# Kernel optimization log

Measured on AMD Instinct MI355X. Metric: run time of the kernel, lower is better.

Reference implementation:

```python
import jax, jax.numpy as jnp
import numpy as np

N = 100000      # nodes
E = 1600000     # edges (before self-loops)
IN_C = 128
HID = 32
HEADS = 4
NEG_SLOPE = 0.2  # PyG GATConv default


def gat_layer(x, W, a_src, a_dst, b, src, dst, n, heads, out_c, concat):
    # x: [n, F_in], W: [F_in, heads*out_c]
    h = (x @ W).reshape(n, heads, out_c)                      # [n, H, C]
    as_n = (h * a_src).sum(-1)                                # [n, H]
    ad_n = (h * a_dst).sum(-1)                                # [n, H]
    e = jax.nn.leaky_relu(as_n[src] + ad_n[dst], NEG_SLOPE)   # [E, H]
    # softmax over incoming edges of each destination node
    m = jax.ops.segment_max(e, dst, num_segments=n)           # [n, H]
    ee = jnp.exp(e - m[dst])
    denom = jax.ops.segment_sum(ee, dst, num_segments=n)      # [n, H]
    alpha = ee / (denom[dst] + 1e-16)                         # [E, H]
    out = jax.ops.segment_sum(h[src] * alpha[:, :, None], dst, num_segments=n)  # [n, H, C]
    out = out.reshape(n, heads * out_c) if concat else out.mean(axis=1)
    return out + b


def setup_inputs() -> dict:
    key = jax.random.key(0)
    ks = jax.random.split(key, 12)
    x = jax.random.normal(ks[0], (N, IN_C), dtype=jnp.float32)
    edge_index = jax.random.randint(ks[1], (2, E), 0, N, dtype=jnp.int64)
    s = 0.1
    return {
        "x": x,
        "edge_index": edge_index,
        "w1": jax.random.normal(ks[2], (IN_C, HEADS * HID), dtype=jnp.float32) * s,
        "a1_src": jax.random.normal(ks[3], (HEADS, HID), dtype=jnp.float32) * s,
        "a1_dst": jax.random.normal(ks[4], (HEADS, HID), dtype=jnp.float32) * s,
        "b1": jnp.zeros((HEADS * HID,), dtype=jnp.float32),
        "w2": jax.random.normal(ks[5], (HEADS * HID, HID), dtype=jnp.float32) * s,
        "a2_src": jax.random.normal(ks[6], (1, HID), dtype=jnp.float32) * s,
        "a2_dst": jax.random.normal(ks[7], (1, HID), dtype=jnp.float32) * s,
        "b2": jnp.zeros((HID,), dtype=jnp.float32),
        "wl": jax.random.normal(ks[8], (HID, 1), dtype=jnp.float32) * s,
        "bl": jnp.zeros((1,), dtype=jnp.float32),
    }


def reference(x, edge_index, w1, a1_src, a1_dst, b1, w2, a2_src, a2_dst, b2, wl, bl):
    n = x.shape[0]
    loop = jnp.arange(n, dtype=edge_index.dtype)
    # PyG GATConv adds self-loops by default
    src = jnp.concatenate([edge_index[0], loop])
    dst = jnp.concatenate([edge_index[1], loop])
    h = jax.nn.elu(gat_layer(x, w1, a1_src, a1_dst, b1, src, dst, n, HEADS, HID, True))
    h = jax.nn.elu(gat_layer(h, w2, a2_src, a2_dst, b2, src, dst, n, 1, HID, False))
    return (h @ wl + bl).squeeze(-1)   # [n]
```

## Files before the change

### kernel.cpp

```cpp
#include <hip/hip_runtime.h>
#include <math.h>

__device__ __forceinline__ float leaky02(float v) { return v > 0.f ? v : 0.2f * v; }
__device__ __forceinline__ float eluf(float v) { return v > 0.f ? v : __expf(v) - 1.f; }
__device__ __forceinline__ float expc(float v) { return __expf(fminf(v, 60.f)); }
__device__ __forceinline__ unsigned short f2bf(float f) {
    unsigned int u = __float_as_uint(f);
    return (unsigned short)((u + 0x7FFFu + ((u >> 16) & 1u)) >> 16);
}
__device__ __forceinline__ float bflo(unsigned int u) { return __uint_as_float(u << 16); }
__device__ __forceinline__ float bfhi(unsigned int u) { return __uint_as_float(u & 0xFFFF0000u); }

__global__ __launch_bounds__(256) void k_init1(int* __restrict__ p, int n) {
    int t = blockIdx.x * 256 + threadIdx.x;
    if (t < n) p[t] = 1;
}

__global__ __launch_bounds__(256, 2) void k_gemm1(
    const float* __restrict__ x, const float* __restrict__ w1,
    const float* __restrict__ a1s, const float* __restrict__ a1d,
    unsigned short* __restrict__ h1b, float* __restrict__ as1, float* __restrict__ ad1, int N)
{
    __shared__ float xs[64 * 128];
    __shared__ float wsh[128 * 64];
    const int half = blockIdx.x & 1;
    const int tile = blockIdx.x >> 1;
    const int tid  = threadIdx.x;
    const int r_base = tile * 64;

    for (int i = tid; i < 2048; i += 256) {
        int k = i >> 4, c4 = i & 15;
        float4 v = *(const float4*)(w1 + k * 128 + half * 64 + c4 * 4);
        *(float4*)(wsh + k * 64 + c4 * 4) = v;
    }
    for (int i = tid; i < 2048; i += 256) {
        int r = i >> 5, k4 = i & 31;
        int rr = r_base + r; if (rr >= N) rr = N - 1;
        float4 v = *(const float4*)(x + (size_t)rr * 128 + k4 * 4);
        *(float4*)(xs + r * 128 + (k4 ^ (r & 7)) * 4) = v;
    }
    __syncthreads();

    const int c0 = (tid & 15) * 4;
    const int r0 = (tid >> 4) * 4;
    const int swz0 = ((r0 + 0) & 7) << 2;
    const int swz1 = ((r0 + 1) & 7) << 2;
    const int swz2 = ((r0 + 2) & 7) << 2;
    const int swz3 = ((r0 + 3) & 7) << 2;
    const float* xb0 = xs + (r0 + 0) * 128;
    const float* xb1 = xs + (r0 + 1) * 128;
    const float* xb2 = xs + (r0 + 2) * 128;
    const float* xb3 = xs + (r0 + 3) * 128;

    float4 acc0 = {0,0,0,0}, acc1 = {0,0,0,0}, acc2 = {0,0,0,0}, acc3 = {0,0,0,0};
#pragma unroll 4
    for (int k = 0; k < 128; ++k) {
        float4 wv = *(const float4*)(wsh + k * 64 + c0);
        float x0 = xb0[k ^ swz0];
        float x1 = xb1[k ^ swz1];
        float x2 = xb2[k ^ swz2];
        float x3 = xb3[k ^ swz3];
        acc0.x = fmaf(x0, wv.x, acc0.x); acc0.y = fmaf(x0, wv.y, acc0.y);
        acc0.z = fmaf(x0, wv.z, acc0.z); acc0.w = fmaf(x0, wv.w, acc0.w);
        acc1.x = fmaf(x1, wv.x, acc1.x); acc1.y = fmaf(x1, wv.y, acc1.y);
        acc1.z = fmaf(x1, wv.z, acc1.z); acc1.w = fmaf(x1, wv.w, acc1.w);
        acc2.x = fmaf(x2, wv.x, acc2.x); acc2.y = fmaf(x2, wv.y, acc2.y);
        acc2.z = fmaf(x2, wv.z, acc2.z); acc2.w = fmaf(x2, wv.w, acc2.w);
        acc3.x = fmaf(x3, wv.x, acc3.x); acc3.y = fmaf(x3, wv.y, acc3.y);
        acc3.z = fmaf(x3, wv.z, acc3.z); acc3.w = fmaf(x3, wv.w, acc3.w);
    }

    const int cg = half * 64 + c0;
    const float4 avs = *(const float4*)(a1s + cg);
    const float4 avd = *(const float4*)(a1d + cg);
    const int head = half * 2 + ((tid & 15) >> 3);
    float4 accs[4] = {acc0, acc1, acc2, acc3};
#pragma unroll
    for (int i = 0; i < 4; ++i) {
        int r = r_base + r0 + i;
        float4 a = accs[i];
        float ps = a.x * avs.x + a.y * avs.y + a.z * avs.z + a.w * avs.w;
        float pd = a.x * avd.x + a.y * avd.y + a.z * avd.z + a.w * avd.w;
        ps += __shfl_xor(ps, 1); pd += __shfl_xor(pd, 1);
        ps += __shfl_xor(ps, 2); pd += __shfl_xor(pd, 2);
        ps += __shfl_xor(ps, 4); pd += __shfl_xor(pd, 4);
        if (r < N) {
            ushort4 hb;
            hb.x = f2bf(a.x); hb.y = f2bf(a.y); hb.z = f2bf(a.z); hb.w = f2bf(a.w);
            *(ushort4*)(h1b + (size_t)r * 128 + cg) = hb;
            if ((tid & 7) == 0) {
                as1[(size_t)r * 4 + head] = ps;
                ad1[(size_t)r * 4 + head] = pd;
            }
        }
    }
}

__global__ __launch_bounds__(256) void k_hist(const int* __restrict__ ei, int* __restrict__ counts,
                                              int E) {
    int t = blockIdx.x * 256 + threadIdx.x;
    if (t >= E) return;
    atomicAdd(&counts[ei[E + t]], 1);
}

__global__ __launch_bounds__(256) void k_bsum(const int* __restrict__ counts,
                                              int* __restrict__ bsum, int N) {
    int t = threadIdx.x;
    int base = blockIdx.x * 1024 + t * 4;
    int s = 0;
    if (base + 3 < N) { int4 v = *(const int4*)(counts + base); s = v.x + v.y + v.z + v.w; }
    else { for (int j = 0; j < 4; ++j) if (base + j < N) s += counts[base + j]; }
#pragma unroll
    for (int off = 1; off < 64; off <<= 1) s += __shfl_xor(s, off);
    __shared__ int wt[4];
    if ((t & 63) == 0) wt[t >> 6] = s;
    __syncthreads();
    if (t == 0) bsum[blockIdx.x] = wt[0] + wt[1] + wt[2] + wt[3];
}

__global__ __launch_bounds__(1024) void k_scansums(const int* __restrict__ bsum,
                                                   int* __restrict__ boff,
                                                   int* __restrict__ rowp_last, int NB) {
    __shared__ int ps[1024];
    int t = threadIdx.x;
    int v = (t < NB) ? bsum[t] : 0;
    ps[t] = v;
    __syncthreads();
    for (int off = 1; off < 1024; off <<= 1) {
        int u = (t >= off) ? ps[t - off] : 0;
        __syncthreads();
        ps[t] += u;
        __syncthreads();
    }
    if (t < NB) boff[t] = ps[t] - v;
    if (t == NB - 1) *rowp_last = ps[t];
}

__global__ __launch_bounds__(256) void k_scatter(const int* __restrict__ counts,
                                                 const int* __restrict__ boff,
                                                 int* __restrict__ rowp, int* __restrict__ pos, int N) {
    int t = threadIdx.x;
    int lane = t & 63, wv = t >> 6;
    int base = blockIdx.x * 1024 + t * 4;
    int c0 = 0, c1 = 0, c2 = 0, c3 = 0;
    if (base + 3 < N) { int4 v = *(const int4*)(counts + base); c0 = v.x; c1 = v.y; c2 = v.z; c3 = v.w; }
    else {
        if (base     < N) c0 = counts[base];
        if (base + 1 < N) c1 = counts[base + 1];
        if (base + 2 < N) c2 = counts[base + 2];
        if (base + 3 < N) c3 = counts[base + 3];
    }
    int ts = c0 + c1 + c2 + c3;
    int inc = ts;
#pragma unroll
    for (int off = 1; off < 64; off <<= 1) { int u = __shfl_up(inc, off); if (lane >= off) inc += u; }
    int excl = inc - ts;
    __shared__ int wt[4];
    if (lane == 63) wt[wv] = inc;
    __syncthreads();
    int woff = 0;
    for (int i = 0; i < wv; ++i) woff += wt[i];
    int p = boff[blockIdx.x] + woff + excl;
    if (base     < N) { rowp[base]     = p; pos[base]     = p; p += c0; }
    if (base + 1 < N) { rowp[base + 1] = p; pos[base + 1] = p; p += c1; }
    if (base + 2 < N) { rowp[base + 2] = p; pos[base + 2] = p; p += c2; }
    if (base + 3 < N) { rowp[base + 3] = p; pos[base + 3] = p; p += c3; }
}

__global__ __launch_bounds__(256) void k_fill(
    const int* __restrict__ ei, int* __restrict__ pos,
    int* __restrict__ col, int* __restrict__ dstv,
    const float* __restrict__ as1, const float* __restrict__ ad1,
    float* __restrict__ ew1, int E, int Et)
{
    int t = blockIdx.x * 256 + threadIdx.x;
    if (t >= Et) return;
    int s, dd;
    if (t < E) { s = ei[t]; dd = ei[E + t]; } else { s = dd = t - E; }
    int p = atomicAdd(&pos[dd], 1);
    col[p] = s;
    dstv[p] = dd;
    float4 a4 = *(const float4*)(as1 + (size_t)s * 4);
    float4 d4 = *(const float4*)(ad1 + (size_t)dd * 4);
    float4 w;
    w.x = expc(leaky02(a4.x + d4.x));
    w.y = expc(leaky02(a4.y + d4.y));
    w.z = expc(leaky02(a4.z + d4.z));
    w.w = expc(leaky02(a4.w + d4.w));
    *(float4*)(ew1 + (size_t)p * 4) = w;
}

__global__ __launch_bounds__(256) void k_agg1(
    const int* __restrict__ rowp, const int* __restrict__ col,
    const float* __restrict__ ew1, const unsigned short* __restrict__ h1b,
    const float* __restrict__ b1, float* __restrict__ out1, int N)
{
    const int lane = threadIdx.x & 63;
    const int wid  = (blockIdx.x * 256 + threadIdx.x) >> 6;
    const int nw   = (gridDim.x * 256) >> 6;
    const int q    = lane >> 4;
    const int cl8  = lane & 15;
    const int hch  = cl8 >> 2;
    for (int n = wid; n < N; n += nw) {
        const int start = rowp[n], end = rowp[n + 1];
        float4 ds = {0.f, 0.f, 0.f, 0.f};
        for (int j = start + lane; j < end; j += 64) {
            float4 w = *(const float4*)(ew1 + (size_t)j * 4);
            ds.x += w.x; ds.y += w.y; ds.z += w.z; ds.w += w.w;
        }
#pragma unroll
        for (int sft = 1; sft < 64; sft <<= 1) {
            ds.x += __shfl_xor(ds.x, sft);
            ds.y += __shfl_xor(ds.y, sft);
            ds.z += __shfl_xor(ds.z, sft);
            ds.w += __shfl_xor(ds.w, sft);
        }
        const float dh = (hch == 0) ? ds.x : (hch == 1) ? ds.y : (hch == 2) ? ds.z : ds.w;
        const float rdh = 1.f / (dh + 1e-16f);
        float acc[8] = {0.f,0.f,0.f,0.f,0.f,0.f,0.f,0.f};
        for (int j = start + q; j < end; j += 4) {
            int s = col[j];
            float alpha = ew1[(size_t)j * 4 + hch] * rdh;
            uint4 hv = *(const uint4*)(h1b + (size_t)s * 128 + cl8 * 8);
            acc[0] = fmaf(alpha, bflo(hv.x), acc[0]);
            acc[1] = fmaf(alpha, bfhi(hv.x), acc[1]);
            acc[2] = fmaf(alpha, bflo(hv.y), acc[2]);
            acc[3] = fmaf(alpha, bfhi(hv.y), acc[3]);
            acc[4] = fmaf(alpha, bflo(hv.z), acc[4]);
            acc[5] = fmaf(alpha, bfhi(hv.z), acc[5]);
            acc[6] = fmaf(alpha, bflo(hv.w), acc[6]);
            acc[7] = fmaf(alpha, bfhi(hv.w), acc[7]);
        }
#pragma unroll
        for (int i = 0; i < 8; ++i) {
            acc[i] += __shfl_xor(acc[i], 16);
            acc[i] += __shfl_xor(acc[i], 32);
        }
        if (q == 0) {
            float4 bv0 = *(const float4*)(b1 + cl8 * 8);
            float4 bv1 = *(const float4*)(b1 + cl8 * 8 + 4);
            float4 o0, o1;
            o0.x = eluf(acc[0] + bv0.x);
            o0.y = eluf(acc[1] + bv0.y);
            o0.z = eluf(acc[2] + bv0.z);
            o0.w = eluf(acc[3] + bv0.w);
            o1.x = eluf(acc[4] + bv1.x);
            o1.y = eluf(acc[5] + bv1.y);
            o1.z = eluf(acc[6] + bv1.z);
            o1.w = eluf(acc[7] + bv1.w);
            *(float4*)(out1 + (size_t)n * 128 + cl8 * 8)     = o0;
            *(float4*)(out1 + (size_t)n * 128 + cl8 * 8 + 4) = o1;
        }
    }
}

__global__ __launch_bounds__(256, 2) void k_gemm2(
    const float* __restrict__ out1, const float* __restrict__ w2,
    const float* __restrict__ a2s, const float* __restrict__ a2d,
    float* __restrict__ z2, float* __restrict__ as2, float* __restrict__ ad2, int N)
{
    __shared__ float xs[128 * 128];
    __shared__ float wsh[128 * 32];
    const int tid = threadIdx.x;
    const int r_base = blockIdx.x * 128;

    for (int i = tid; i < 1024; i += 256) {
        int k = i >> 3, c4 = i & 7;
        float4 v = *(const float4*)(w2 + k * 32 + c4 * 4);
        *(float4*)(wsh + k * 32 + c4 * 4) = v;
    }
    for (int i = tid; i < 4096; i += 256) {
        int r = i >> 5, k4 = i & 31;
        int rr = r_base + r; if (rr >= N) rr = N - 1;
        float4 v = *(const float4*)(out1 + (size_t)rr * 128 + k4 * 4);
        *(float4*)(xs + r * 128 + (k4 ^ (r & 7)) * 4) = v;
    }
    __syncthreads();

    const int c0 = (tid & 7) * 4;
    const int r0 = (tid >> 3) * 4;
    const int swz0 = ((r0 + 0) & 7) << 2;
    const int swz1 = ((r0 + 1) & 7) << 2;
    const int swz2 = ((r0 + 2) & 7) << 2;
    const int swz3 = ((r0 + 3) & 7) << 2;
    const float* xb0 = xs + (r0 + 0) * 128;
    const float* xb1 = xs + (r0 + 1) * 128;
    const float* xb2 = xs + (r0 + 2) * 128;
    const float* xb3 = xs + (r0 + 3) * 128;

    float4 acc0 = {0,0,0,0}, acc1 = {0,0,0,0}, acc2 = {0,0,0,0}, acc3 = {0,0,0,0};
#pragma unroll 4
    for (int k = 0; k < 128; ++k) {
        float4 wv = *(const float4*)(wsh + k * 32 + c0);
        float x0 = xb0[k ^ swz0];
        float x1 = xb1[k ^ swz1];
        float x2 = xb2[k ^ swz2];
        float x3 = xb3[k ^ swz3];
        acc0.x = fmaf(x0, wv.x, acc0.x); acc0.y = fmaf(x0, wv.y, acc0.y);
        acc0.z = fmaf(x0, wv.z, acc0.z); acc0.w = fmaf(x0, wv.w, acc0.w);
        acc1.x = fmaf(x1, wv.x, acc1.x); acc1.y = fmaf(x1, wv.y, acc1.y);
        acc1.z = fmaf(x1, wv.z, acc1.z); acc1.w = fmaf(x1, wv.w, acc1.w);
        acc2.x = fmaf(x2, wv.x, acc2.x); acc2.y = fmaf(x2, wv.y, acc2.y);
        acc2.z = fmaf(x2, wv.z, acc2.z); acc2.w = fmaf(x2, wv.w, acc2.w);
        acc3.x = fmaf(x3, wv.x, acc3.x); acc3.y = fmaf(x3, wv.y, acc3.y);
        acc3.z = fmaf(x3, wv.z, acc3.z); acc3.w = fmaf(x3, wv.w, acc3.w);
    }

    const float4 avs = *(const float4*)(a2s + c0);
    const float4 avd = *(const float4*)(a2d + c0);
    float4 accs[4] = {acc0, acc1, acc2, acc3};
#pragma unroll
    for (int i = 0; i < 4; ++i) {
        int r = r_base + r0 + i;
        float4 a = accs[i];
        float ps = a.x * avs.x + a.y * avs.y + a.z * avs.z + a.w * avs.w;
        float pd = a.x * avd.x + a.y * avd.y + a.z * avd.z + a.w * avd.w;
        ps += __shfl_xor(ps, 1); pd += __shfl_xor(pd, 1);
        ps += __shfl_xor(ps, 2); pd += __shfl_xor(pd, 2);
        ps += __shfl_xor(ps, 4); pd += __shfl_xor(pd, 4);
        if (r < N) {
            *(float4*)(z2 + (size_t)r * 32 + c0) = a;
            if ((tid & 7) == 0) { as2[r] = ps; ad2[r] = pd; }
        }
    }
}

__global__ __launch_bounds__(256) void k_ew2(
    const int* __restrict__ col, const int* __restrict__ dstv,
    const float* __restrict__ as2, const float* __restrict__ ad2,
    float* __restrict__ ew2, int Et)
{
    int t = blockIdx.x * 256 + threadIdx.x;
    if (t >= Et) return;
    int s = col[t], dd = dstv[t];
    ew2[t] = expc(leaky02(as2[s] + ad2[dd]));
}

__global__ __launch_bounds__(256) void k_agg2(
    const int* __restrict__ rowp, const int* __restrict__ col,
    const float* __restrict__ ew2, const float* __restrict__ z2,
    const float* __restrict__ b2, const float* __restrict__ wl,
    const float* __restrict__ bl, float* __restrict__ out, int N)
{
    const int lane = threadIdx.x & 63;
    const int wid  = (blockIdx.x * 256 + threadIdx.x) >> 6;
    const int nw   = (gridDim.x * 256) >> 6;
    const int q  = lane >> 4;
    const int cl = lane & 15;
    for (int n = wid; n < N; n += nw) {
        const int start = rowp[n], end = rowp[n + 1];
        float d = 0.f;
        for (int j = start + lane; j < end; j += 64) d += ew2[j];
#pragma unroll
        for (int sft = 1; sft < 64; sft <<= 1) d += __shfl_xor(d, sft);
        const float rd = 1.f / (d + 1e-16f);
        float2 acc = {0.f, 0.f};
        for (int j = start + q; j < end; j += 4) {
            int s = col[j];
            float alpha = ew2[j] * rd;
            float2 zv = *(const float2*)(z2 + (size_t)s * 32 + cl * 2);
            acc.x = fmaf(alpha, zv.x, acc.x);
            acc.y = fmaf(alpha, zv.y, acc.y);
        }
        acc.x += __shfl_xor(acc.x, 16); acc.y += __shfl_xor(acc.y, 16);
        acc.x += __shfl_xor(acc.x, 32); acc.y += __shfl_xor(acc.y, 32);
        float h0 = eluf(acc.x + b2[cl * 2]);
        float h1v = eluf(acc.y + b2[cl * 2 + 1]);
        float p = h0 * wl[cl * 2] + h1v * wl[cl * 2 + 1];
#pragma unroll
        for (int sft = 1; sft < 16; sft <<= 1) p += __shfl_xor(p, sft);
        if (lane == 0) out[n] = p + bl[0];
    }
}

extern "C" void kernel_launch(void* const* d_in, const int* in_sizes, int n_in,
                              void* d_out, int out_size, void* d_ws, size_t ws_size,
                              hipStream_t stream) {
    const float* x   = (const float*)d_in[0];
    const int*   ei  = (const int*)d_in[1];
    const float* w1  = (const float*)d_in[2];
    const float* a1s = (const float*)d_in[3];
    const float* a1d = (const float*)d_in[4];
    const float* b1  = (const float*)d_in[5];
    const float* w2  = (const float*)d_in[6];
    const float* a2s = (const float*)d_in[7];
    const float* a2d = (const float*)d_in[8];
    const float* b2  = (const float*)d_in[9];
    const float* wl  = (const float*)d_in[10];
    const float* bl  = (const float*)d_in[11];
    float* out = (float*)d_out;

    const int N  = in_sizes[0] / 128;
    const int E  = in_sizes[1] / 2;
    const int Et = E + N;
    const int NB = (N + 1023) / 1024;

    float* ws   = (float*)d_ws;
    unsigned short* h1b = (unsigned short*)ws;
    float* out1 = ws   + (size_t)N * 64;
    float* ew1  = out1 + (size_t)N * 128;
    float* as1  = ew1  + (size_t)Et * 4;
    float* ad1  = as1  + (size_t)N * 4;
    float* z2   = ad1  + (size_t)N * 4;
    float* as2  = z2   + (size_t)N * 32;
    float* ad2  = as2  + N;
    int* counts = (int*)(ad2 + N);
    int* rowp   = counts + N;
    int* col    = rowp + (N + 1);
    int* pos    = col + Et;
    int* bsum   = pos + N;
    int* boff   = bsum + NB;
    int* dstv   = boff + NB;
    float* ew2  = ew1;

    k_init1<<<(N + 255) / 256, 256, 0, stream>>>(counts, N);
    k_gemm1<<<2 * ((N + 63) / 64), 256, 0, stream>>>(x, w1, a1s, a1d, h1b, as1, ad1, N);
    k_hist<<<(E + 255) / 256, 256, 0, stream>>>(ei, counts, E);
    k_bsum<<<NB, 256, 0, stream>>>(counts, bsum, N);
    k_scansums<<<1, 1024, 0, stream>>>(bsum, boff, rowp + N, NB);
    k_scatter<<<NB, 256, 0, stream>>>(counts, boff, rowp, pos, N);
    k_fill<<<(Et + 255) / 256, 256, 0, stream>>>(ei, pos, col, dstv, as1, ad1, ew1, E, Et);
    k_agg1<<<4096, 256, 0, stream>>>(rowp, col, ew1, h1b, b1, out1, N);
    k_gemm2<<<(N + 127) / 128, 256, 0, stream>>>(out1, w2, a2s, a2d, z2, as2, ad2, N);
    k_ew2<<<(Et + 255) / 256, 256, 0, stream>>>(col, dstv, as2, ad2, ew2, Et);
    k_agg2<<<4096, 256, 0, stream>>>(rowp, col, ew2, z2, b2, wl, bl, out, N);
}
```

Before: 578.3 us.

## Recompute attention edge weights inside aggregation kernels instead of materializing them

Edge attention scores are no longer precomputed and stored per edge. For layer 1, the fill kernel stops writing the dstv and ew1 arrays. For layer 2, the separate k_ew2 kernel is removed. Both aggregation kernels now gather the per-source attention logit and recompute exp(leaky_relu(as+ad)) on the fly, in both the denominator pass and the weighted-sum pass. This removes large per-edge writes and reads plus one kernel launch, at the cost of redundant exp work and extra random gathers of as1/as2 per edge.

Result: no change. 575.8 us (-0.4%).

```diff
diff --git a/kernel.cpp b/kernel.cpp
--- a/kernel.cpp
+++ b/kernel.cpp
@@ -169,9 +169,7 @@
 
 __global__ __launch_bounds__(256) void k_fill(
     const int* __restrict__ ei, int* __restrict__ pos,
-    int* __restrict__ col, int* __restrict__ dstv,
-    const float* __restrict__ as1, const float* __restrict__ ad1,
-    float* __restrict__ ew1, int E, int Et)
+    int* __restrict__ col, int E, int Et)
 {
     int t = blockIdx.x * 256 + threadIdx.x;
     if (t >= Et) return;
@@ -179,20 +177,12 @@
     if (t < E) { s = ei[t]; dd = ei[E + t]; } else { s = dd = t - E; }
     int p = atomicAdd(&pos[dd], 1);
     col[p] = s;
-    dstv[p] = dd;
-    float4 a4 = *(const float4*)(as1 + (size_t)s * 4);
-    float4 d4 = *(const float4*)(ad1 + (size_t)dd * 4);
-    float4 w;
-    w.x = expc(leaky02(a4.x + d4.x));
-    w.y = expc(leaky02(a4.y + d4.y));
-    w.z = expc(leaky02(a4.z + d4.z));
-    w.w = expc(leaky02(a4.w + d4.w));
-    *(float4*)(ew1 + (size_t)p * 4) = w;
 }
 
 __global__ __launch_bounds__(256) void k_agg1(
     const int* __restrict__ rowp, const int* __restrict__ col,
-    const float* __restrict__ ew1, const unsigned short* __restrict__ h1b,
+    const float* __restrict__ as1, const float* __restrict__ ad1,
+    const unsigned short* __restrict__ h1b,
     const float* __restrict__ b1, float* __restrict__ out1, int N)
 {
     const int lane = threadIdx.x & 63;
@@ -203,10 +193,15 @@
     const int hch  = cl8 >> 2;
     for (int n = wid; n < N; n += nw) {
         const int start = rowp[n], end = rowp[n + 1];
+        const float4 ad4 = *(const float4*)(ad1 + (size_t)n * 4);
         float4 ds = {0.f, 0.f, 0.f, 0.f};
         for (int j = start + lane; j < end; j += 64) {
-            float4 w = *(const float4*)(ew1 + (size_t)j * 4);
-            ds.x += w.x; ds.y += w.y; ds.z += w.z; ds.w += w.w;
+            int s = col[j];
+            float4 a4 = *(const float4*)(as1 + (size_t)s * 4);
+            ds.x += expc(leaky02(a4.x + ad4.x));
+            ds.y += expc(leaky02(a4.y + ad4.y));
+            ds.z += expc(leaky02(a4.z + ad4.z));
+            ds.w += expc(leaky02(a4.w + ad4.w));
         }
 #pragma unroll
         for (int sft = 1; sft < 64; sft <<= 1) {
@@ -215,12 +210,14 @@
             ds.z += __shfl_xor(ds.z, sft);
             ds.w += __shfl_xor(ds.w, sft);
         }
-        const float dh = (hch == 0) ? ds.x : (hch == 1) ? ds.y : (hch == 2) ? ds.z : ds.w;
+        const float dh  = (hch == 0) ? ds.x : (hch == 1) ? ds.y : (hch == 2) ? ds.z : ds.w;
+        const float adh = (hch == 0) ? ad4.x : (hch == 1) ? ad4.y : (hch == 2) ? ad4.z : ad4.w;
         const float rdh = 1.f / (dh + 1e-16f);
         float acc[8] = {0.f,0.f,0.f,0.f,0.f,0.f,0.f,0.f};
         for (int j = start + q; j < end; j += 4) {
             int s = col[j];
-            float alpha = ew1[(size_t)j * 4 + hch] * rdh;
+            float asv = as1[(size_t)s * 4 + hch];
+            float alpha = expc(leaky02(asv + adh)) * rdh;
             uint4 hv = *(const uint4*)(h1b + (size_t)s * 128 + cl8 * 8);
             acc[0] = fmaf(alpha, bflo(hv.x), acc[0]);
             acc[1] = fmaf(alpha, bfhi(hv.x), acc[1]);
@@ -325,22 +322,12 @@
     }
 }
 
-__global__ __launch_bounds__(256) void k_ew2(
-    const int* __restrict__ col, const int* __restrict__ dstv,
-    const float* __restrict__ as2, const float* __restrict__ ad2,
-    float* __restrict__ ew2, int Et)
-{
-    int t = blockIdx.x * 256 + threadIdx.x;
-    if (t >= Et) return;
-    int s = col[t], dd = dstv[t];
-    ew2[t] = expc(leaky02(as2[s] + ad2[dd]));
-}
-
 __global__ __launch_bounds__(256) void k_agg2(
     const int* __restrict__ rowp, const int* __restrict__ col,
-    const float* __restrict__ ew2, const float* __restrict__ z2,
-    const float* __restrict__ b2, const float* __restrict__ wl,
-    const float* __restrict__ bl, float* __restrict__ out, int N)
+    const float* __restrict__ as2, const float* __restrict__ ad2,
+    const float* __restrict__ z2, const float* __restrict__ b2,
+    const float* __restrict__ wl, const float* __restrict__ bl,
+    float* __restrict__ out, int N)
 {
     const int lane = threadIdx.x & 63;
     const int wid  = (blockIdx.x * 256 + threadIdx.x) >> 6;
@@ -349,15 +336,19 @@
     const int cl = lane & 15;
     for (int n = wid; n < N; n += nw) {
         const int start = rowp[n], end = rowp[n + 1];
+        const float adn = ad2[n];
         float d = 0.f;
-        for (int j = start + lane; j < end; j += 64) d += ew2[j];
+        for (int j = start + lane; j < end; j += 64) {
+            int s = col[j];
+            d += expc(leaky02(as2[s] + adn));
+        }
 #pragma unroll
         for (int sft = 1; sft < 64; sft <<= 1) d += __shfl_xor(d, sft);
         const float rd = 1.f / (d + 1e-16f);
         float2 acc = {0.f, 0.f};
         for (int j = start + q; j < end; j += 4) {
             int s = col[j];
-            float alpha = ew2[j] * rd;
+            float alpha = expc(leaky02(as2[s] + adn)) * rd;
             float2 zv = *(const float2*)(z2 + (size_t)s * 32 + cl * 2);
             acc.x = fmaf(alpha, zv.x, acc.x);
             acc.y = fmaf(alpha, zv.y, acc.y);
@@ -398,8 +389,7 @@
     float* ws   = (float*)d_ws;
     unsigned short* h1b = (unsigned short*)ws;
     float* out1 = ws   + (size_t)N * 64;
-    float* ew1  = out1 + (size_t)N * 128;
-    float* as1  = ew1  + (size_t)Et * 4;
+    float* as1  = out1 + (size_t)N * 128;
     float* ad1  = as1  + (size_t)N * 4;
     float* z2   = ad1  + (size_t)N * 4;
     float* as2  = z2   + (size_t)N * 32;
@@ -410,8 +400,6 @@
     int* pos    = col + Et;
     int* bsum   = pos + N;
     int* boff   = bsum + NB;
-    int* dstv   = boff + NB;
-    float* ew2  = ew1;
 
     k_init1<<<(N + 255) / 256, 256, 0, stream>>>(counts, N);
     k_gemm1<<<2 * ((N + 63) / 64), 256, 0, stream>>>(x, w1, a1s, a1d, h1b, as1, ad1, N);
@@ -419,9 +407,8 @@
     k_bsum<<<NB, 256, 0, stream>>>(counts, bsum, N);
     k_scansums<<<1, 1024, 0, stream>>>(bsum, boff, rowp + N, NB);
     k_scatter<<<NB, 256, 0, stream>>>(counts, boff, rowp, pos, N);
-    k_fill<<<(Et + 255) / 256, 256, 0, stream>>>(ei, pos, col, dstv, as1, ad1, ew1, E, Et);
-    k_agg1<<<4096, 256, 0, stream>>>(rowp, col, ew1, h1b, b1, out1, N);
+    k_fill<<<(Et + 255) / 256, 256, 0, stream>>>(ei, pos, col, E, Et);
+    k_agg1<<<4096, 256, 0, stream>>>(rowp, col, as1, ad1, h1b, b1, out1, N);
     k_gemm2<<<(N + 127) / 128, 256, 0, stream>>>(out1, w2, a2s, a2d, z2, as2, ad2, N);
-    k_ew2<<<(Et + 255) / 256, 256, 0, stream>>>(col, dstv, as2, ad2, ew2, Et);
-    k_agg2<<<4096, 256, 0, stream>>>(rowp, col, ew2, z2, b2, wl, bl, out, N);
-}
+    k_agg2<<<4096, 256, 0, stream>>>(rowp, col, as2, ad2, z2, b2, wl, bl, out, N);
+}
```
